# Performance work log

Hardware: AMD Instinct MI355X
Metric: run time of the kernel (lower is better)

Reference implementation:

```python
import jax, jax.numpy as jnp
import numpy as np

B, T = 16, 2048
OBS_DIM, ACT_DIM, HIDDEN = 64, 16, 512


def setup_inputs() -> dict:
    key = jax.random.key(0)
    ks = jax.random.split(key, 6)
    n = lambda k, shape, scale: (jax.random.normal(k, shape, dtype=jnp.float32) * scale)
    return {
        "obs": n(ks[0], (B, T, OBS_DIM), 1.0),
        "act": n(ks[1], (B, T, ACT_DIM), 1.0),
        "W_e": n(ks[2], (HIDDEN, OBS_DIM + ACT_DIM), 0.05),   # embed Linear weight
        "b_e": jnp.zeros((HIDDEN,), jnp.float32),             # embed Linear bias
        "a_raw": n(ks[3], (HIDDEN,), 0.5),                    # diagonal decay (pre-tanh)
        "W_B": n(ks[4], (HIDDEN, HIDDEN), 0.02),              # B Linear weight (no bias)
        "W_out": n(ks[5], (OBS_DIM, HIDDEN), 0.04),           # out Linear weight
        "b_out": jnp.zeros((OBS_DIM,), jnp.float32),          # out Linear bias
    }


def reference(obs, act, W_e, b_e, a_raw, W_B, W_out, b_out):
    # x: [B, T, obs+act]
    x = jnp.concatenate([obs, act], axis=-1)
    # embed: Linear + ReLU, batched over all timesteps -> u: [B, T, H]
    u = jax.nn.relu(jnp.einsum('btd,hd->bth', x, W_e) + b_e)
    # B projection batched over all t (the per-step matmul in the torch loop)
    v = jnp.einsum('bth,gh->btg', u, W_B)  # [B, T, H]
    a = jnp.tanh(a_raw)  # [H]
    # Diagonal linear recurrence s_t = a * s_{t-1} + v_t, s_0 starting from zeros,
    # realized as a parallel (log-depth) associative scan over (decay, input) pairs.
    A = jnp.broadcast_to(a, v.shape)
    def combine(c1, c2):
        a1, b1 = c1
        a2, b2 = c2
        return (a1 * a2, a2 * b1 + b2)
    _, s = jax.lax.associative_scan(combine, (A, v), axis=1)  # s: [B, T, H]
    # out projection per step -> preds: [B, T, obs_dim]
    return jnp.einsum('bth,oh->bto', s, W_out) + b_out
```

## Files before the change

### kernel.cpp

```cpp
#include <hip/hip_runtime.h>
#include <hip/hip_bf16.h>

#define B_    16
#define T_    2048
#define H_    512
#define BT_   32768
#define DIN   80
#define L_    64
#define C_    32
#define O_    64
#define NCHUNK (BT_ / L_)

typedef __attribute__((ext_vector_type(8))) short short8;
typedef __attribute__((ext_vector_type(4))) float f32x4;
typedef __attribute__((ext_vector_type(4))) float float4v;

__device__ __forceinline__ float bf2f(unsigned short u) {
  union { unsigned int i; float f; } x; x.i = ((unsigned int)u) << 16; return x.f;
}
__device__ __forceinline__ unsigned short f2bf(float f) {
  union { float f; unsigned int i; } x; x.f = f;
  unsigned int r = x.i + 0x7fffu + ((x.i >> 16) & 1u);
  return (unsigned short)(r >> 16);
}

#define WB_N  (H_ * H_)
#define WO_N  (O_ * H_)

__global__ __launch_bounds__(512) void embed_gemm(
    const float* __restrict__ obs, const float* __restrict__ act,
    const float* __restrict__ W_e, const float* __restrict__ b_e,
    const float* __restrict__ a_raw, const float* __restrict__ W_B,
    const float* __restrict__ W_out,
    unsigned short* __restrict__ WBb, unsigned short* __restrict__ Woutb,
    float* __restrict__ aarr, float* __restrict__ powa,
    unsigned short* __restrict__ u)
{
  __shared__ __align__(16) unsigned char lds[131072];

  const int tid  = threadIdx.x;
  const int lane = tid & 63;
  const int wid  = tid >> 6;
  const int wr   = wid >> 2;
  const int wc   = wid & 3;
  const int cl   = lane & 15;
  const int kgrp = lane >> 4;
  const int rg   = kgrp * 4;

  const int X  = (int)blockIdx.x & 7;
  const int j  = (int)blockIdx.x >> 3;
  const int mt = X * 16 + (j >> 1);
  const int nt = j & 1;
  const int row0 = mt * 256, col0 = nt * 256;

  {
    const int g = (int)blockIdx.x * 512 + tid;
    #pragma unroll
    for (int r = 0; r < 2; ++r) {
      const int idx = g * 2 + r;
      WBb[idx] = f2bf(W_B[idx]);
    }
    if (g < WO_N) Woutb[g] = f2bf(W_out[g]);
    if (g < H_) {
      const float a = tanhf(a_raw[g]);
      aarr[g] = a;
      float p = a;
      #pragma unroll
      for (int i = 0; i < 16; ++i) { powa[i * H_ + g] = p; p *= a; }
    }
  }

  {
    const int row  = tid >> 1;
    const int half = tid & 1;
    {
      const float4v* src = (const float4v*)(obs + (size_t)(row0 + row) * 64 + half * 32);
      float f[32];
      #pragma unroll
      for (int i = 0; i < 8; ++i) {
        const float4v t4 = src[i];
        f[i*4+0]=t4[0]; f[i*4+1]=t4[1]; f[i*4+2]=t4[2]; f[i*4+3]=t4[3];
      }
      #pragma unroll
      for (int cc = 0; cc < 4; ++cc) {
        short8 o8;
        #pragma unroll
        for (int jj = 0; jj < 8; ++jj) o8[jj] = (short)f2bf(f[cc*8+jj]);
        const int c16 = half * 4 + cc;
        *(short8*)(lds + row * 128 + ((c16 ^ (row & 7)) << 4)) = o8;
      }
    }
    {
      short8 z8;
      #pragma unroll
      for (int jj = 0; jj < 8; ++jj) z8[jj] = 0;
      if (half == 0) {
        const float4v* asrc = (const float4v*)(act + (size_t)(row0 + row) * 16);
        float g2[16];
        #pragma unroll
        for (int i = 0; i < 4; ++i) {
          const float4v t4 = asrc[i];
          g2[i*4+0]=t4[0]; g2[i*4+1]=t4[1]; g2[i*4+2]=t4[2]; g2[i*4+3]=t4[3];
        }
        #pragma unroll
        for (int cc = 0; cc < 2; ++cc) {
          short8 o8;
          #pragma unroll
          for (int jj = 0; jj < 8; ++jj) o8[jj] = (short)f2bf(g2[cc*8+jj]);
          *(short8*)(lds + 65536 + row * 128 + ((cc ^ (row & 7)) << 4)) = o8;
        }
        #pragma unroll
        for (int cc = 2; cc < 4; ++cc)
          *(short8*)(lds + 65536 + row * 128 + ((cc ^ (row & 7)) << 4)) = z8;
      } else {
        #pragma unroll
        for (int cc = 4; cc < 8; ++cc)
          *(short8*)(lds + 65536 + row * 128 + ((cc ^ (row & 7)) << 4)) = z8;
      }
    }
  }
  {
    const int colL = tid >> 1;
    const int col  = col0 + colL;
    const int half = tid & 1;
    {
      const float4v* src = (const float4v*)(W_e + (size_t)col * DIN + half * 32);
      float f[32];
      #pragma unroll
      for (int i = 0; i < 8; ++i) {
        const float4v t4 = src[i];
        f[i*4+0]=t4[0]; f[i*4+1]=t4[1]; f[i*4+2]=t4[2]; f[i*4+3]=t4[3];
      }
      #pragma unroll
      for (int cc = 0; cc < 4; ++cc) {
        short8 o8;
        #pragma unroll
        for (int jj = 0; jj < 8; ++jj) o8[jj] = (short)f2bf(f[cc*8+jj]);
        const int c16 = half * 4 + cc;
        *(short8*)(lds + 32768 + colL * 128 + ((c16 ^ (colL & 7)) << 4)) = o8;
      }
    }
    {
      short8 z8;
      #pragma unroll
      for (int jj = 0; jj < 8; ++jj) z8[jj] = 0;
      if (half == 0) {
        const float4v* src = (const float4v*)(W_e + (size_t)col * DIN + 64);
        float g2[16];
        #pragma unroll
        for (int i = 0; i < 4; ++i) {
          const float4v t4 = src[i];
          g2[i*4+0]=t4[0]; g2[i*4+1]=t4[1]; g2[i*4+2]=t4[2]; g2[i*4+3]=t4[3];
        }
        #pragma unroll
        for (int cc = 0; cc < 2; ++cc) {
          short8 o8;
          #pragma unroll
          for (int jj = 0; jj < 8; ++jj) o8[jj] = (short)f2bf(g2[cc*8+jj]);
          *(short8*)(lds + 98304 + colL * 128 + ((cc ^ (colL & 7)) << 4)) = o8;
        }
        #pragma unroll
        for (int cc = 2; cc < 4; ++cc)
          *(short8*)(lds + 98304 + colL * 128 + ((cc ^ (colL & 7)) << 4)) = z8;
      } else {
        #pragma unroll
        for (int cc = 4; cc < 8; ++cc)
          *(short8*)(lds + 98304 + colL * 128 + ((cc ^ (colL & 7)) << 4)) = z8;
      }
    }
  }
  __syncthreads();

  f32x4 acc[8][4];
  #pragma unroll
  for (int m = 0; m < 8; ++m)
    #pragma unroll
    for (int n = 0; n < 4; ++n) acc[m][n] = f32x4{0.f, 0.f, 0.f, 0.f};

  #pragma unroll
  for (int q = 0; q < 2; ++q) {
    const unsigned char* bufp = lds + q * 65536;
    short8 bfr[4][2];
    #pragma unroll
    for (int n = 0; n < 4; ++n) {
      const int col = wc * 64 + n * 16 + cl;
      #pragma unroll
      for (int ks = 0; ks < 2; ++ks)
        bfr[n][ks] = *(const short8*)(bufp + 32768 + col * 128 +
                                      ((((ks << 2) + kgrp) ^ (col & 7)) << 4));
    }
    #pragma unroll
    for (int g = 0; g < 4; ++g) {
      short8 af[2][2];
      #pragma unroll
      for (int mm = 0; mm < 2; ++mm) {
        const int row = wr * 128 + (g * 2 + mm) * 16 + cl;
        #pragma unroll
        for (int ks = 0; ks < 2; ++ks)
          af[mm][ks] = *(const short8*)(bufp + row * 128 +
                                        ((((ks << 2) + kgrp) ^ (row & 7)) << 4));
      }
      #pragma unroll
      for (int ks = 0; ks < 2; ++ks)
        #pragma unroll
        for (int mm = 0; mm < 2; ++mm)
          #pragma unroll
          for (int n = 0; n < 4; ++n)
            acc[g * 2 + mm][n] = __builtin_amdgcn_mfma_f32_16x16x32_bf16(
                af[mm][ks], bfr[n][ks], acc[g * 2 + mm][n], 0, 0, 0);
    }
  }

  #pragma unroll
  for (int m = 0; m < 8; ++m) {
    #pragma unroll
    for (int n = 0; n < 4; ++n) {
      const int gc = col0 + wc * 64 + n * 16 + cl;
      const float be = b_e[gc];
      #pragma unroll
      for (int e2 = 0; e2 < 4; ++e2) {
        const int gr = row0 + wr * 128 + m * 16 + rg + e2;
        u[(size_t)gr * H_ + gc] = f2bf(fmaxf(acc[m][n][e2] + be, 0.f));
      }
    }
  }
}

__global__ __launch_bounds__(512) void gemm_bproj(
    const unsigned short* __restrict__ A, const unsigned short* __restrict__ Bt,
    unsigned short* __restrict__ Cb,
    const float* __restrict__ powa, float* __restrict__ e)
{
  constexpr int NT = 8;
  __shared__ __align__(16) unsigned char lds[131072];

  const int tid  = threadIdx.x;
  const int lane = tid & 63;
  const int wid  = tid >> 6;
  const int wr   = wid >> 2;
  const int wc   = wid & 3;
  const int cl   = lane & 15;
  const int kgrp = lane >> 4;
  const int rg   = kgrp * 4;

  const int X  = (int)blockIdx.x & 7;
  const int j  = (int)blockIdx.x >> 3;
  const int mt = X * 16 + (j >> 1);
  const int nt = j & 1;
  const int row0 = mt * 256, col0 = nt * 256;

  auto stageA = [&](int q, int buf) {
    const int k0 = q * 64;
    #pragma unroll
    for (int r = 0; r < 4; ++r) {
      const int o   = r * 8192 + tid * 16;
      const int row = o >> 7;
      const int c16 = (o >> 4) & 7;
      const int kk  = (c16 ^ (row & 7)) << 3;
      __builtin_amdgcn_global_load_lds(
          (const __attribute__((address_space(1))) void*)
              (A + (size_t)(row0 + row) * H_ + k0 + kk),
          (__attribute__((address_space(3))) void*)(lds + buf * 65536 + o),
          16, 0, 0);
    }
  };
  auto stageB_round = [&](int q, int buf, int r) {
    const int k0 = q * 64;
    const int o   = r * 8192 + tid * 16;
    const int col = o >> 7;
    const int c16 = (o >> 4) & 7;
    const int kk  = (c16 ^ (col & 7)) << 3;
    __builtin_amdgcn_global_load_lds(
        (const __attribute__((address_space(1))) void*)
            (Bt + (size_t)(col0 + col) * H_ + k0 + kk),
        (__attribute__((address_space(3))) void*)(lds + buf * 65536 + 32768 + o),
        16, 0, 0);
  };

  f32x4 acc[8][4];
  #pragma unroll
  for (int m = 0; m < 8; ++m)
    #pragma unroll
    for (int n = 0; n < 4; ++n) acc[m][n] = f32x4{0.f, 0.f, 0.f, 0.f};

  stageA(0, 0);
  #pragma unroll
  for (int r = 0; r < 4; ++r) stageB_round(0, 0, r);
  #pragma unroll
  for (int r = 0; r < 4; ++r) stageB_round(1, 1, r);
  asm volatile("s_waitcnt vmcnt(4)" ::: "memory");
  __builtin_amdgcn_sched_barrier(0);
  __builtin_amdgcn_s_barrier();

  for (int q = 0; q < NT; ++q) {
    const int cur = q & 1;
    const unsigned char* bufp = lds + cur * 65536;

    if (q + 1 < NT) stageA(q + 1, cur ^ 1);

    short8 bfr[4][2];
    #pragma unroll
    for (int n = 0; n < 4; ++n) {
      const int col = wc * 64 + n * 16 + cl;
      #pragma unroll
      for (int ks = 0; ks < 2; ++ks)
        bfr[n][ks] = *(const short8*)(bufp + 32768 + col * 128 +
                                      ((((ks << 2) + kgrp) ^ (col & 7)) << 4));
    }
    asm volatile("s_waitcnt lgkmcnt(0)" ::: "memory");
    __builtin_amdgcn_sched_barrier(0);
    __builtin_amdgcn_s_barrier();

    __builtin_amdgcn_s_setprio(1);
    #pragma unroll
    for (int g = 0; g < 4; ++g) {
      if (q + 2 < NT) stageB_round(q + 2, cur, g);
      short8 af[2][2];
      #pragma unroll
      for (int mm = 0; mm < 2; ++mm) {
        const int row = wr * 128 + (g * 2 + mm) * 16 + cl;
        #pragma unroll
        for (int ks = 0; ks < 2; ++ks)
          af[mm][ks] = *(const short8*)(bufp + row * 128 +
                                        ((((ks << 2) + kgrp) ^ (row & 7)) << 4));
      }
      #pragma unroll
      for (int ks = 0; ks < 2; ++ks)
        #pragma unroll
        for (int mm = 0; mm < 2; ++mm)
          #pragma unroll
          for (int n = 0; n < 4; ++n)
            acc[g * 2 + mm][n] = __builtin_amdgcn_mfma_f32_16x16x32_bf16(
                af[mm][ks], bfr[n][ks], acc[g * 2 + mm][n], 0, 0, 0);
    }
    __builtin_amdgcn_s_setprio(0);

    if (q + 2 < NT) {
      asm volatile("s_waitcnt vmcnt(4)" ::: "memory");
    } else if (q + 1 < NT) {
      asm volatile("s_waitcnt vmcnt(0)" ::: "memory");
    }
    __builtin_amdgcn_sched_barrier(0);
    __builtin_amdgcn_s_barrier();
  }

  #pragma unroll
  for (int m = 0; m < 8; ++m) {
    #pragma unroll
    for (int n = 0; n < 4; ++n) {
      const int gc = col0 + wc * 64 + n * 16 + cl;
      #pragma unroll
      for (int e2 = 0; e2 < 4; ++e2) {
        const int gr = row0 + wr * 128 + m * 16 + rg + e2;
        Cb[(size_t)gr * H_ + gc] = f2bf(acc[m][n][e2]);
      }
    }
  }

  #pragma unroll
  for (int c = 0; c < 2; ++c) {
    const int chunk = ((row0 + wr * 128) >> 6) + c;
    #pragma unroll
    for (int n = 0; n < 4; ++n) {
      const int h = col0 + wc * 64 + n * 16 + cl;
      const float a16 = powa[15 * H_ + h];
      float ep = 0.f;
      #pragma unroll
      for (int e2 = 0; e2 < 4; ++e2) {
        const int k = 15 - rg - e2;
        const float wk = (k == 0) ? 1.f : powa[(size_t)(k - 1) * H_ + h];
        float hsum = acc[c * 4 + 0][n][e2];
        hsum = fmaf(hsum, a16, acc[c * 4 + 1][n][e2]);
        hsum = fmaf(hsum, a16, acc[c * 4 + 2][n][e2]);
        hsum = fmaf(hsum, a16, acc[c * 4 + 3][n][e2]);
        ep = fmaf(wk, hsum, ep);
      }
      ep += __shfl_xor(ep, 16);
      ep += __shfl_xor(ep, 32);
      if (kgrp == 0)
        e[(size_t)chunk * H_ + h] = ep;
    }
  }
}

__global__ __launch_bounds__(256) void scan_out(
    const unsigned int* __restrict__ v, const float* __restrict__ e,
    const float* __restrict__ aarr, const unsigned short* __restrict__ Wo,
    const float* __restrict__ b_out, float* __restrict__ y)
{
  __shared__ __align__(16) unsigned char sbytes[64 * 1024];
  const int blk = blockIdx.x;
  const int b = blk >> 5, c = blk & 31;
  const int tid = threadIdx.x;
  const int lane = tid & 63, w = tid >> 6;
  const int row_base = blk * L_;

  {
    const int h0 = tid * 2;
    const float a0 = aarr[h0], a1 = aarr[h0 + 1];
    float aL0 = a0 * a0, aL1 = a1 * a1;
    aL0 *= aL0; aL1 *= aL1;
    aL0 *= aL0; aL1 *= aL1;
    aL0 *= aL0; aL1 *= aL1;
    aL0 *= aL0; aL1 *= aL1;
    aL0 *= aL0; aL1 *= aL1;
    float s0 = 0.f, s1 = 0.f;
    #pragma unroll
    for (int g = 0; g < 4; ++g) {
      float ev0[8], ev1[8];
      #pragma unroll
      for (int k = 0; k < 8; ++k) {
        const size_t o = ((size_t)(b * C_ + g * 8 + k)) * H_ + h0;
        ev0[k] = e[o]; ev1[k] = e[o + 1];
      }
      #pragma unroll
      for (int k = 0; k < 8; ++k) {
        const bool pred = (g * 8 + k) < c;
        s0 = pred ? fmaf(aL0, s0, ev0[k]) : s0;
        s1 = pred ? fmaf(aL1, s1, ev1[k]) : s1;
      }
    }
    const unsigned int* vp = v + (size_t)row_base * (H_ / 2) + tid;
    #pragma unroll 8
    for (int t = 0; t < L_; ++t) {
      const unsigned int pv = vp[(size_t)t * (H_ / 2)];
      s0 = fmaf(a0, s0, bf2f((unsigned short)(pv & 0xffff)));
      s1 = fmaf(a1, s1, bf2f((unsigned short)(pv >> 16)));
      const int byte = t * 1024 + ((tid * 4) ^ ((t & 7) << 4));
      *(unsigned int*)(sbytes + byte) =
          (unsigned int)f2bf(s0) | ((unsigned int)f2bf(s1) << 16);
    }
  }
  __syncthreads();

  f32x4 acc[4];
  #pragma unroll
  for (int n = 0; n < 4; ++n) acc[n] = f32x4{0.f, 0.f, 0.f, 0.f};
  const int r = w * 16 + (lane & 15);
  const int kof = (lane >> 4) * 8;
  #pragma unroll 4
  for (int k0 = 0; k0 < H_; k0 += 32) {
    const int byte = r * 1024 + (((k0 + kof) * 2) ^ ((r & 7) << 4));
    const short8 af = *(const short8*)(sbytes + byte);
    #pragma unroll
    for (int n = 0; n < 4; ++n) {
      const short8 bf = *(const short8*)(Wo + (size_t)(n * 16 + (lane & 15)) * H_ + k0 + kof);
      acc[n] = __builtin_amdgcn_mfma_f32_16x16x32_bf16(af, bf, acc[n], 0, 0, 0);
    }
  }
  const int cl = lane & 15, rg = (lane >> 4) * 4;
  #pragma unroll
  for (int n = 0; n < 4; ++n) {
    #pragma unroll
    for (int e2 = 0; e2 < 4; ++e2) {
      const int gr = row_base + w * 16 + rg + e2;
      const int gc = n * 16 + cl;
      y[(size_t)gr * O_ + gc] = acc[n][e2] + b_out[gc];
    }
  }
}

extern "C" void kernel_launch(void* const* d_in, const int* in_sizes, int n_in,
                              void* d_out, int out_size, void* d_ws, size_t ws_size,
                              hipStream_t stream)
{
  const float* obs   = (const float*)d_in[0];
  const float* act   = (const float*)d_in[1];
  const float* W_e   = (const float*)d_in[2];
  const float* b_e   = (const float*)d_in[3];
  const float* a_raw = (const float*)d_in[4];
  const float* W_B   = (const float*)d_in[5];
  const float* W_out = (const float*)d_in[6];
  const float* b_out = (const float*)d_in[7];
  float* y = (float*)d_out;

  char* w = (char*)d_ws;
  auto carve = [&](size_t bytes) {
    char* p = w; w += (bytes + 255) & ~(size_t)255; return p;
  };
  unsigned short* WBb   = (unsigned short*)carve((size_t)H_ * H_ * 2);
  unsigned short* Woutb = (unsigned short*)carve((size_t)O_ * H_ * 2);
  float*          aarr  = (float*)carve((size_t)H_ * 4);
  float*          powa  = (float*)carve((size_t)16 * H_ * 4);
  unsigned short* u     = (unsigned short*)carve((size_t)BT_ * H_ * 2);
  unsigned short* v     = (unsigned short*)carve((size_t)BT_ * H_ * 2);
  float*          e     = (float*)carve((size_t)NCHUNK * H_ * 4);

  embed_gemm<<<256, 512, 0, stream>>>(obs, act, W_e, b_e, a_raw, W_B, W_out,
                                      WBb, Woutb, aarr, powa, u);
  gemm_bproj<<<256, 512, 0, stream>>>(u, WBb, v, powa, e);
  scan_out<<<NCHUNK, 256, 0, stream>>>((const unsigned int*)v, e, aarr,
                                       Woutb, b_out, y);
}
```

Baseline: 68.21 us.

## Fuse B-projection, chunked scan and output projection with cross-block flag chaining

Merges the B-projection GEMM, the diagonal recurrence and the output projection into one kernel. Each block scans its 256-row tile in registers using shuffles, publishes a slab carry, and waits on flags from earlier slabs of the same batch before applying the carry-in. It then multiplies the tile by its half of W_out and writes split-K partials, which a small kernel sums with the bias. This removes the round trip of the bf16 v tensor and the separate scan kernel. In exchange it adds inter-block spin-waiting, which assumes the predecessor blocks are co-resident, plus extra partial-output traffic and a memset.

```diff
diff --git a/kernel.cpp b/kernel.cpp
--- a/kernel.cpp
+++ b/kernel.cpp
@@ -9,7 +9,7 @@
 #define L_    64
 #define C_    32
 #define O_    64
-#define NCHUNK (BT_ / L_)
+#define NSLAB 128
 
 typedef __attribute__((ext_vector_type(8))) short short8;
 typedef __attribute__((ext_vector_type(4))) float f32x4;
@@ -226,10 +226,11 @@
   }
 }
 
-__global__ __launch_bounds__(512) void gemm_bproj(
-    const unsigned short* __restrict__ A, const unsigned short* __restrict__ Bt,
-    unsigned short* __restrict__ Cb,
-    const float* __restrict__ powa, float* __restrict__ e)
+__global__ __launch_bounds__(512) void bproj_scan_out(
+    const unsigned short* __restrict__ u, const unsigned short* __restrict__ WBb,
+    const unsigned short* __restrict__ Woutb, const float* __restrict__ aarr,
+    const float* __restrict__ powa, float* __restrict__ Eslab,
+    int* __restrict__ flags, float* __restrict__ yp0, float* __restrict__ yp1)
 {
   constexpr int NT = 8;
   __shared__ __align__(16) unsigned char lds[131072];
@@ -241,7 +242,6 @@
   const int wc   = wid & 3;
   const int cl   = lane & 15;
   const int kgrp = lane >> 4;
-  const int rg   = kgrp * 4;
 
   const int X  = (int)blockIdx.x & 7;
   const int j  = (int)blockIdx.x >> 3;
@@ -259,7 +259,7 @@
       const int kk  = (c16 ^ (row & 7)) << 3;
       __builtin_amdgcn_global_load_lds(
           (const __attribute__((address_space(1))) void*)
-              (A + (size_t)(row0 + row) * H_ + k0 + kk),
+              (u + (size_t)(row0 + row) * H_ + k0 + kk),
           (__attribute__((address_space(3))) void*)(lds + buf * 65536 + o),
           16, 0, 0);
     }
@@ -272,7 +272,7 @@
     const int kk  = (c16 ^ (col & 7)) << 3;
     __builtin_amdgcn_global_load_lds(
         (const __attribute__((address_space(1))) void*)
-            (Bt + (size_t)(col0 + col) * H_ + k0 + kk),
+            (WBb + (size_t)(col0 + col) * H_ + k0 + kk),
         (__attribute__((address_space(3))) void*)(lds + buf * 65536 + 32768 + o),
         16, 0, 0);
   };
@@ -344,120 +344,181 @@
     __builtin_amdgcn_s_barrier();
   }
 
-  #pragma unroll
-  for (int m = 0; m < 8; ++m) {
+  float Cn[4];
+  #pragma unroll
+  for (int n = 0; n < 4; ++n) {
+    const int h = col0 + wc * 64 + n * 16 + cl;
+    const float a1  = aarr[h];
+    const float pe0 = powa[0 * H_ + h];
+    const float pe1 = powa[1 * H_ + h];
+    const float pe2 = powa[2 * H_ + h];
+    const float pe3 = powa[3 * H_ + h];
+    const float a8  = powa[7 * H_ + h];
+    const float a16 = powa[15 * H_ + h];
+    const float aw0 = powa[(4 * kgrp + 0) * H_ + h];
+    const float aw1 = powa[(4 * kgrp + 1) * H_ + h];
+    const float aw2 = powa[(4 * kgrp + 2) * H_ + h];
+    const float aw3 = powa[(4 * kgrp + 3) * H_ + h];
+    float C = 0.f;
+    #pragma unroll
+    for (int m = 0; m < 8; ++m) {
+      acc[m][n][1] = fmaf(a1, acc[m][n][0], acc[m][n][1]);
+      acc[m][n][2] = fmaf(a1, acc[m][n][1], acc[m][n][2]);
+      acc[m][n][3] = fmaf(a1, acc[m][n][2], acc[m][n][3]);
+      float P = acc[m][n][3];
+      const float t1 = __shfl_up(P, 16, 64);
+      if (kgrp >= 1) P = fmaf(pe3, t1, P);
+      const float t2 = __shfl_up(P, 32, 64);
+      if (kgrp >= 2) P = fmaf(a8, t2, P);
+      float Xc = __shfl_up(P, 16, 64);
+      if (kgrp == 0) Xc = 0.f;
+      const float bt = __shfl(P, (lane & 15) + 48, 64);
+      acc[m][n][0] = fmaf(pe0, Xc, fmaf(aw0, C, acc[m][n][0]));
+      acc[m][n][1] = fmaf(pe1, Xc, fmaf(aw1, C, acc[m][n][1]));
+      acc[m][n][2] = fmaf(pe2, Xc, fmaf(aw2, C, acc[m][n][2]));
+      acc[m][n][3] = fmaf(pe3, Xc, fmaf(aw3, C, acc[m][n][3]));
+      C = fmaf(a16, C, bt);
+    }
+    Cn[n] = C;
+  }
+
+  float* E128 = (float*)lds;
+  if (kgrp == 0) {
+    #pragma unroll
+    for (int n = 0; n < 4; ++n)
+      E128[wr * 256 + wc * 64 + n * 16 + cl] = Cn[n];
+  }
+  __syncthreads();
+  {
+    if (wr == 0 && kgrp == 0) {
+      #pragma unroll
+      for (int n = 0; n < 4; ++n) {
+        const int hl = wc * 64 + n * 16 + cl;
+        const int h = col0 + hl;
+        const float a16 = powa[15 * H_ + h];
+        const float a32 = a16 * a16, a64 = a32 * a32, a128 = a64 * a64;
+        Eslab[(size_t)mt * H_ + h] = fmaf(a128, E128[hl], E128[256 + hl]);
+      }
+    }
+  }
+  __threadfence();
+  __syncthreads();
+  if (tid == 0)
+    __hip_atomic_store(&flags[mt * 2 + nt], 1, __ATOMIC_RELEASE,
+                       __HIP_MEMORY_SCOPE_AGENT);
+  const int bs = mt & ~7;
+  const int npred = mt - bs;
+  if (tid < npred) {
+    while (__hip_atomic_load(&flags[(bs + tid) * 2 + nt], __ATOMIC_ACQUIRE,
+                             __HIP_MEMORY_SCOPE_AGENT) == 0)
+      __builtin_amdgcn_s_sleep(2);
+  }
+  __syncthreads();
+
+  #pragma unroll
+  for (int n = 0; n < 4; ++n) {
+    const int hl = wc * 64 + n * 16 + cl;
+    const int h = col0 + hl;
+    const float a16 = powa[15 * H_ + h];
+    const float a32 = a16 * a16, a64 = a32 * a32;
+    const float a128 = a64 * a64, a256 = a128 * a128;
+    float S = 0.f;
+    for (int mp = bs; mp < mt; ++mp) {
+      const float ev = __hip_atomic_load(&Eslab[(size_t)mp * H_ + h],
+                                         __ATOMIC_RELAXED,
+                                         __HIP_MEMORY_SCOPE_AGENT);
+      S = fmaf(a256, S, ev);
+    }
+    const float Ch = (wr == 0) ? S : fmaf(a128, S, E128[hl]);
+    const float aw0 = powa[(4 * kgrp + 0) * H_ + h];
+    const float aw1 = powa[(4 * kgrp + 1) * H_ + h];
+    const float aw2 = powa[(4 * kgrp + 2) * H_ + h];
+    const float aw3 = powa[(4 * kgrp + 3) * H_ + h];
+    float coef = 1.f;
+    #pragma unroll
+    for (int m = 0; m < 8; ++m) {
+      const float cc = coef * Ch;
+      acc[m][n][0] = fmaf(aw0, cc, acc[m][n][0]);
+      acc[m][n][1] = fmaf(aw1, cc, acc[m][n][1]);
+      acc[m][n][2] = fmaf(aw2, cc, acc[m][n][2]);
+      acc[m][n][3] = fmaf(aw3, cc, acc[m][n][3]);
+      coef *= a16;
+    }
+  }
+  __syncthreads();
+
+  #pragma unroll
+  for (int n = 0; n < 4; ++n) {
+    const int h2 = (wc * 64 + n * 16 + cl) * 2;
+    #pragma unroll
+    for (int m = 0; m < 8; ++m) {
+      const int tb = wr * 128 + m * 16 + kgrp * 4;
+      #pragma unroll
+      for (int e2 = 0; e2 < 4; ++e2) {
+        const int t = tb + e2;
+        *(unsigned short*)(lds + t * 512 + (h2 ^ ((t & 7) << 4))) =
+            f2bf(acc[m][n][e2]);
+      }
+    }
+  }
+  __syncthreads();
+
+  f32x4 oacc[2][4];
+  #pragma unroll
+  for (int mo = 0; mo < 2; ++mo)
+    #pragma unroll
+    for (int n = 0; n < 4; ++n) oacc[mo][n] = f32x4{0.f, 0.f, 0.f, 0.f};
+
+  #pragma unroll
+  for (int ks = 0; ks < 8; ++ks) {
+    const int k0 = ks * 32 + kgrp * 8;
+    short8 af[2];
+    #pragma unroll
+    for (int mo = 0; mo < 2; ++mo) {
+      const int t = wid * 32 + mo * 16 + cl;
+      af[mo] = *(const short8*)(lds + t * 512 + ((k0 * 2) ^ ((t & 7) << 4)));
+    }
     #pragma unroll
     for (int n = 0; n < 4; ++n) {
-      const int gc = col0 + wc * 64 + n * 16 + cl;
+      const short8 bf = *(const short8*)(Woutb + (size_t)(n * 16 + cl) * H_ +
+                                         col0 + k0);
+      #pragma unroll
+      for (int mo = 0; mo < 2; ++mo)
+        oacc[mo][n] = __builtin_amdgcn_mfma_f32_16x16x32_bf16(
+            af[mo], bf, oacc[mo][n], 0, 0, 0);
+    }
+  }
+
+  float* yp = nt ? yp1 : yp0;
+  #pragma unroll
+  for (int mo = 0; mo < 2; ++mo) {
+    #pragma unroll
+    for (int n = 0; n < 4; ++n) {
       #pragma unroll
       for (int e2 = 0; e2 < 4; ++e2) {
-        const int gr = row0 + wr * 128 + m * 16 + rg + e2;
-        Cb[(size_t)gr * H_ + gc] = f2bf(acc[m][n][e2]);
-      }
-    }
-  }
-
-  #pragma unroll
-  for (int c = 0; c < 2; ++c) {
-    const int chunk = ((row0 + wr * 128) >> 6) + c;
-    #pragma unroll
-    for (int n = 0; n < 4; ++n) {
-      const int h = col0 + wc * 64 + n * 16 + cl;
-      const float a16 = powa[15 * H_ + h];
-      float ep = 0.f;
-      #pragma unroll
-      for (int e2 = 0; e2 < 4; ++e2) {
-        const int k = 15 - rg - e2;
-        const float wk = (k == 0) ? 1.f : powa[(size_t)(k - 1) * H_ + h];
-        float hsum = acc[c * 4 + 0][n][e2];
-        hsum = fmaf(hsum, a16, acc[c * 4 + 1][n][e2]);
-        hsum = fmaf(hsum, a16, acc[c * 4 + 2][n][e2]);
-        hsum = fmaf(hsum, a16, acc[c * 4 + 3][n][e2]);
-        ep = fmaf(wk, hsum, ep);
-      }
-      ep += __shfl_xor(ep, 16);
-      ep += __shfl_xor(ep, 32);
-      if (kgrp == 0)
-        e[(size_t)chunk * H_ + h] = ep;
+        const int gr = row0 + wid * 32 + mo * 16 + kgrp * 4 + e2;
+        const int gc = n * 16 + cl;
+        yp[(size_t)gr * O_ + gc] = oacc[mo][n][e2];
+      }
     }
   }
 }
 
-__global__ __launch_bounds__(256) void scan_out(
-    const unsigned int* __restrict__ v, const float* __restrict__ e,
-    const float* __restrict__ aarr, const unsigned short* __restrict__ Wo,
+__global__ __launch_bounds__(256) void ysum(
+    const float* __restrict__ yp0, const float* __restrict__ yp1,
     const float* __restrict__ b_out, float* __restrict__ y)
 {
-  __shared__ __align__(16) unsigned char sbytes[64 * 1024];
-  const int blk = blockIdx.x;
-  const int b = blk >> 5, c = blk & 31;
-  const int tid = threadIdx.x;
-  const int lane = tid & 63, w = tid >> 6;
-  const int row_base = blk * L_;
-
-  {
-    const int h0 = tid * 2;
-    const float a0 = aarr[h0], a1 = aarr[h0 + 1];
-    float aL0 = a0 * a0, aL1 = a1 * a1;
-    aL0 *= aL0; aL1 *= aL1;
-    aL0 *= aL0; aL1 *= aL1;
-    aL0 *= aL0; aL1 *= aL1;
-    aL0 *= aL0; aL1 *= aL1;
-    aL0 *= aL0; aL1 *= aL1;
-    float s0 = 0.f, s1 = 0.f;
-    #pragma unroll
-    for (int g = 0; g < 4; ++g) {
-      float ev0[8], ev1[8];
-      #pragma unroll
-      for (int k = 0; k < 8; ++k) {
-        const size_t o = ((size_t)(b * C_ + g * 8 + k)) * H_ + h0;
-        ev0[k] = e[o]; ev1[k] = e[o + 1];
-      }
-      #pragma unroll
-      for (int k = 0; k < 8; ++k) {
-        const bool pred = (g * 8 + k) < c;
-        s0 = pred ? fmaf(aL0, s0, ev0[k]) : s0;
-        s1 = pred ? fmaf(aL1, s1, ev1[k]) : s1;
-      }
-    }
-    const unsigned int* vp = v + (size_t)row_base * (H_ / 2) + tid;
-    #pragma unroll 8
-    for (int t = 0; t < L_; ++t) {
-      const unsigned int pv = vp[(size_t)t * (H_ / 2)];
-      s0 = fmaf(a0, s0, bf2f((unsigned short)(pv & 0xffff)));
-      s1 = fmaf(a1, s1, bf2f((unsigned short)(pv >> 16)));
-      const int byte = t * 1024 + ((tid * 4) ^ ((t & 7) << 4));
-      *(unsigned int*)(sbytes + byte) =
-          (unsigned int)f2bf(s0) | ((unsigned int)f2bf(s1) << 16);
-    }
-  }
-  __syncthreads();
-
-  f32x4 acc[4];
-  #pragma unroll
-  for (int n = 0; n < 4; ++n) acc[n] = f32x4{0.f, 0.f, 0.f, 0.f};
-  const int r = w * 16 + (lane & 15);
-  const int kof = (lane >> 4) * 8;
-  #pragma unroll 4
-  for (int k0 = 0; k0 < H_; k0 += 32) {
-    const int byte = r * 1024 + (((k0 + kof) * 2) ^ ((r & 7) << 4));
-    const short8 af = *(const short8*)(sbytes + byte);
-    #pragma unroll
-    for (int n = 0; n < 4; ++n) {
-      const short8 bf = *(const short8*)(Wo + (size_t)(n * 16 + (lane & 15)) * H_ + k0 + kof);
-      acc[n] = __builtin_amdgcn_mfma_f32_16x16x32_bf16(af, bf, acc[n], 0, 0, 0);
-    }
-  }
-  const int cl = lane & 15, rg = (lane >> 4) * 4;
-  #pragma unroll
-  for (int n = 0; n < 4; ++n) {
-    #pragma unroll
-    for (int e2 = 0; e2 < 4; ++e2) {
-      const int gr = row_base + w * 16 + rg + e2;
-      const int gc = n * 16 + cl;
-      y[(size_t)gr * O_ + gc] = acc[n][e2] + b_out[gc];
-    }
-  }
+  const int g = blockIdx.x * 256 + threadIdx.x;
+  const int i4 = g * 4;
+  const float4v p0 = ((const float4v*)yp0)[g];
+  const float4v p1 = ((const float4v*)yp1)[g];
+  const float4v bb = *(const float4v*)(b_out + (i4 & 63));
+  float4v o;
+  o[0] = p0[0] + p1[0] + bb[0];
+  o[1] = p0[1] + p1[1] + bb[1];
+  o[2] = p0[2] + p1[2] + bb[2];
+  o[3] = p0[3] + p1[3] + bb[3];
+  ((float4v*)y)[g] = o;
 }
 
 extern "C" void kernel_launch(void* const* d_in, const int* in_sizes, int n_in,
@@ -483,12 +544,16 @@
   float*          aarr  = (float*)carve((size_t)H_ * 4);
   float*          powa  = (float*)carve((size_t)16 * H_ * 4);
   unsigned short* u     = (unsigned short*)carve((size_t)BT_ * H_ * 2);
-  unsigned short* v     = (unsigned short*)carve((size_t)BT_ * H_ * 2);
-  float*          e     = (float*)carve((size_t)NCHUNK * H_ * 4);
+  float*          Eslab = (float*)carve((size_t)NSLAB * H_ * 4);
+  int*            flags = (int*)carve((size_t)NSLAB * 2 * 4);
+  float*          yp0   = (float*)carve((size_t)BT_ * O_ * 4);
+  float*          yp1   = (float*)carve((size_t)BT_ * O_ * 4);
+
+  hipMemsetAsync(flags, 0, (size_t)NSLAB * 2 * 4, stream);
 
   embed_gemm<<<256, 512, 0, stream>>>(obs, act, W_e, b_e, a_raw, W_B, W_out,
                                       WBb, Woutb, aarr, powa, u);
-  gemm_bproj<<<256, 512, 0, stream>>>(u, WBb, v, powa, e);
-  scan_out<<<NCHUNK, 256, 0, stream>>>((const unsigned int*)v, e, aarr,
-                                       Woutb, b_out, y);
+  bproj_scan_out<<<256, 512, 0, stream>>>(u, WBb, Woutb, aarr, powa,
+                                          Eslab, flags, yp0, yp1);
+  ysum<<<(BT_ * O_ / 4) / 256, 256, 0, stream>>>(yp0, yp1, b_out, y);
 }
```

Result: slower. 102.8 us (+50.8%).

## Shrink B-projection GEMM tiles to 128x256 with K=32 steps for more blocks

Applied to the files above, without the earlier changes.

The B-projection GEMM now uses 128-row M tiles and 32-wide K steps, which doubles the grid to 512 blocks and shrinks LDS to 48KB per block. Launch bounds now request 4 blocks per CU. The swizzle pattern, the staging split and the per-chunk end-state reduction are reworked to match. The aim is better occupancy and CU coverage, traded against lower per-block operand reuse, twice as many K iterations and barriers, and more global traffic for the shared B operand.

```diff
diff --git a/kernel.cpp b/kernel.cpp
--- a/kernel.cpp
+++ b/kernel.cpp
@@ -226,13 +226,15 @@
   }
 }
 
-__global__ __launch_bounds__(512) void gemm_bproj(
+__global__ __launch_bounds__(512, 4) void gemm_bproj(
     const unsigned short* __restrict__ A, const unsigned short* __restrict__ Bt,
     unsigned short* __restrict__ Cb,
     const float* __restrict__ powa, float* __restrict__ e)
 {
-  constexpr int NT = 8;
-  __shared__ __align__(16) unsigned char lds[131072];
+  constexpr int NT = 16;
+  constexpr int ABYTES = 128 * 32 * 2;
+  constexpr int TOT = ABYTES + 256 * 32 * 2;
+  __shared__ __align__(16) unsigned char lds[2 * TOT];
 
   const int tid  = threadIdx.x;
   const int lane = tid & 63;
@@ -245,67 +247,60 @@
 
   const int X  = (int)blockIdx.x & 7;
   const int j  = (int)blockIdx.x >> 3;
-  const int mt = X * 16 + (j >> 1);
+  const int mt = X * 32 + (j >> 1);
   const int nt = j & 1;
-  const int row0 = mt * 256, col0 = nt * 256;
+  const int row0 = mt * 128, col0 = nt * 256;
 
   auto stageA = [&](int q, int buf) {
-    const int k0 = q * 64;
-    #pragma unroll
-    for (int r = 0; r < 4; ++r) {
-      const int o   = r * 8192 + tid * 16;
-      const int row = o >> 7;
-      const int c16 = (o >> 4) & 7;
-      const int kk  = (c16 ^ (row & 7)) << 3;
-      __builtin_amdgcn_global_load_lds(
-          (const __attribute__((address_space(1))) void*)
-              (A + (size_t)(row0 + row) * H_ + k0 + kk),
-          (__attribute__((address_space(3))) void*)(lds + buf * 65536 + o),
-          16, 0, 0);
-    }
+    const int k0 = q * 32;
+    const int o   = tid * 16;
+    const int row = o >> 6;
+    const int c16 = (o >> 4) & 3;
+    const int kk  = (c16 ^ ((row >> 1) & 3)) << 3;
+    __builtin_amdgcn_global_load_lds(
+        (const __attribute__((address_space(1))) void*)
+            (A + (size_t)(row0 + row) * H_ + k0 + kk),
+        (__attribute__((address_space(3))) void*)(lds + buf * TOT + o),
+        16, 0, 0);
   };
   auto stageB_round = [&](int q, int buf, int r) {
-    const int k0 = q * 64;
+    const int k0 = q * 32;
     const int o   = r * 8192 + tid * 16;
-    const int col = o >> 7;
-    const int c16 = (o >> 4) & 7;
-    const int kk  = (c16 ^ (col & 7)) << 3;
+    const int col = o >> 6;
+    const int c16 = (o >> 4) & 3;
+    const int kk  = (c16 ^ ((col >> 1) & 3)) << 3;
     __builtin_amdgcn_global_load_lds(
         (const __attribute__((address_space(1))) void*)
             (Bt + (size_t)(col0 + col) * H_ + k0 + kk),
-        (__attribute__((address_space(3))) void*)(lds + buf * 65536 + 32768 + o),
+        (__attribute__((address_space(3))) void*)(lds + buf * TOT + ABYTES + o),
         16, 0, 0);
   };
 
-  f32x4 acc[8][4];
-  #pragma unroll
-  for (int m = 0; m < 8; ++m)
+  f32x4 acc[4][4];
+  #pragma unroll
+  for (int m = 0; m < 4; ++m)
     #pragma unroll
     for (int n = 0; n < 4; ++n) acc[m][n] = f32x4{0.f, 0.f, 0.f, 0.f};
 
   stageA(0, 0);
-  #pragma unroll
-  for (int r = 0; r < 4; ++r) stageB_round(0, 0, r);
-  #pragma unroll
-  for (int r = 0; r < 4; ++r) stageB_round(1, 1, r);
-  asm volatile("s_waitcnt vmcnt(4)" ::: "memory");
+  stageB_round(0, 0, 0); stageB_round(0, 0, 1);
+  stageB_round(1, 1, 0); stageB_round(1, 1, 1);
+  asm volatile("s_waitcnt vmcnt(2)" ::: "memory");
   __builtin_amdgcn_sched_barrier(0);
   __builtin_amdgcn_s_barrier();
 
   for (int q = 0; q < NT; ++q) {
     const int cur = q & 1;
-    const unsigned char* bufp = lds + cur * 65536;
+    const unsigned char* bufp = lds + cur * TOT;
 
     if (q + 1 < NT) stageA(q + 1, cur ^ 1);
 
-    short8 bfr[4][2];
+    short8 bfr[4];
     #pragma unroll
     for (int n = 0; n < 4; ++n) {
       const int col = wc * 64 + n * 16 + cl;
-      #pragma unroll
-      for (int ks = 0; ks < 2; ++ks)
-        bfr[n][ks] = *(const short8*)(bufp + 32768 + col * 128 +
-                                      ((((ks << 2) + kgrp) ^ (col & 7)) << 4));
+      bfr[n] = *(const short8*)(bufp + ABYTES + col * 64 +
+                                ((kgrp ^ ((col >> 1) & 3)) << 4));
     }
     asm volatile("s_waitcnt lgkmcnt(0)" ::: "memory");
     __builtin_amdgcn_sched_barrier(0);
@@ -314,29 +309,20 @@
     __builtin_amdgcn_s_setprio(1);
     #pragma unroll
     for (int g = 0; g < 4; ++g) {
-      if (q + 2 < NT) stageB_round(q + 2, cur, g);
-      short8 af[2][2];
-      #pragma unroll
-      for (int mm = 0; mm < 2; ++mm) {
-        const int row = wr * 128 + (g * 2 + mm) * 16 + cl;
-        #pragma unroll
-        for (int ks = 0; ks < 2; ++ks)
-          af[mm][ks] = *(const short8*)(bufp + row * 128 +
-                                        ((((ks << 2) + kgrp) ^ (row & 7)) << 4));
-      }
-      #pragma unroll
-      for (int ks = 0; ks < 2; ++ks)
-        #pragma unroll
-        for (int mm = 0; mm < 2; ++mm)
-          #pragma unroll
-          for (int n = 0; n < 4; ++n)
-            acc[g * 2 + mm][n] = __builtin_amdgcn_mfma_f32_16x16x32_bf16(
-                af[mm][ks], bfr[n][ks], acc[g * 2 + mm][n], 0, 0, 0);
+      if ((g == 0 || g == 2) && q + 2 < NT)
+        stageB_round(q + 2, cur, g >> 1);
+      const int row = wr * 64 + g * 16 + cl;
+      const short8 af = *(const short8*)(bufp + row * 64 +
+                                         ((kgrp ^ ((row >> 1) & 3)) << 4));
+      #pragma unroll
+      for (int n = 0; n < 4; ++n)
+        acc[g][n] = __builtin_amdgcn_mfma_f32_16x16x32_bf16(
+            af, bfr[n], acc[g][n], 0, 0, 0);
     }
     __builtin_amdgcn_s_setprio(0);
 
     if (q + 2 < NT) {
-      asm volatile("s_waitcnt vmcnt(4)" ::: "memory");
+      asm volatile("s_waitcnt vmcnt(2)" ::: "memory");
     } else if (q + 1 < NT) {
       asm volatile("s_waitcnt vmcnt(0)" ::: "memory");
     }
@@ -345,21 +331,20 @@
   }
 
   #pragma unroll
-  for (int m = 0; m < 8; ++m) {
+  for (int m = 0; m < 4; ++m) {
     #pragma unroll
     for (int n = 0; n < 4; ++n) {
       const int gc = col0 + wc * 64 + n * 16 + cl;
       #pragma unroll
       for (int e2 = 0; e2 < 4; ++e2) {
-        const int gr = row0 + wr * 128 + m * 16 + rg + e2;
+        const int gr = row0 + wr * 64 + m * 16 + rg + e2;
         Cb[(size_t)gr * H_ + gc] = f2bf(acc[m][n][e2]);
       }
     }
   }
 
-  #pragma unroll
-  for (int c = 0; c < 2; ++c) {
-    const int chunk = ((row0 + wr * 128) >> 6) + c;
+  {
+    const int chunk = mt * 2 + wr;
     #pragma unroll
     for (int n = 0; n < 4; ++n) {
       const int h = col0 + wc * 64 + n * 16 + cl;
@@ -369,10 +354,10 @@
       for (int e2 = 0; e2 < 4; ++e2) {
         const int k = 15 - rg - e2;
         const float wk = (k == 0) ? 1.f : powa[(size_t)(k - 1) * H_ + h];
-        float hsum = acc[c * 4 + 0][n][e2];
-        hsum = fmaf(hsum, a16, acc[c * 4 + 1][n][e2]);
-        hsum = fmaf(hsum, a16, acc[c * 4 + 2][n][e2]);
-        hsum = fmaf(hsum, a16, acc[c * 4 + 3][n][e2]);
+        float hsum = acc[0][n][e2];
+        hsum = fmaf(hsum, a16, acc[1][n][e2]);
+        hsum = fmaf(hsum, a16, acc[2][n][e2]);
+        hsum = fmaf(hsum, a16, acc[3][n][e2]);
         ep = fmaf(wk, hsum, ep);
       }
       ep += __shfl_xor(ep, 16);
@@ -488,7 +473,7 @@
 
   embed_gemm<<<256, 512, 0, stream>>>(obs, act, W_e, b_e, a_raw, W_B, W_out,
                                       WBb, Woutb, aarr, powa, u);
-  gemm_bproj<<<256, 512, 0, stream>>>(u, WBb, v, powa, e);
+  gemm_bproj<<<512, 512, 0, stream>>>(u, WBb, v, powa, e);
   scan_out<<<NCHUNK, 256, 0, stream>>>((const unsigned int*)v, e, aarr,
                                        Woutb, b_out, y);
 }
```

After: 71.33 us. +4.6%, slower.
